# Kernel tuning notes

Hardware: AMD Instinct MI355X
Metric: run time of the kernel (lower is better)

## Reference

```python
import jax, jax.numpy as jnp
import numpy as np

NEG_INF = -1e30


def setup_inputs() -> dict:
    key = jax.random.key(0)
    kq, kk, kv, ks = jax.random.split(key, 4)
    B, H, S, D = 2, 16, 2048, 64
    return {
        "q": jax.random.normal(kq, (B, H, S, D), dtype=jnp.float32),
        "k": jax.random.normal(kk, (B, H, S, D), dtype=jnp.float32),
        "v": jax.random.normal(kv, (B, H, S, D), dtype=jnp.float32),
        "sink_weights": jax.random.normal(ks, (H,), dtype=jnp.float32),
        "sliding_window": 1024,
    }


def reference(q, k, v, sink_weights, sliding_window):
    """Sliding-window causal attention with a learnable attention-sink logit.

    Equivalent to FlexAttention.forward with sink_weights given: an extra kv
    position (the sink) is appended whose score is replaced by sink_weights[h]
    and whose value is zero -> it only adds mass to the softmax denominator.
    """
    B, H, S_q, D = q.shape
    S_kv = k.shape[2]
    scale = 1.0 / np.sqrt(D)

    # [B, H, S_q, S_kv] raw scores
    scores = jnp.einsum("bhqd,bhkd->bhqk", q, k) * scale

    q_idx = jnp.arange(S_q)[:, None]
    kv_idx = jnp.arange(S_kv)[None, :]
    keep = (kv_idx <= q_idx) & (q_idx - kv_idx <= sliding_window)  # [S_q, S_kv]
    scores = jnp.where(keep[None, None], scores, NEG_INF)

    # sink column: per-head learnable logit, always visible
    sink_col = jnp.broadcast_to(
        sink_weights[None, :, None, None], (B, H, S_q, 1)
    )
    logits = jnp.concatenate([scores, sink_col], axis=-1)  # [B,H,S_q,S_kv+1]

    probs = jax.nn.softmax(logits, axis=-1)
    # sink value is zero, so only the first S_kv prob columns hit v
    out = jnp.einsum("bhqk,bhkd->bhqd", probs[..., :S_kv], v)
    return out
```

## Files before the change

### kernel.cpp

```cpp
#include <hip/hip_runtime.h>


typedef __bf16 bf16x8 __attribute__((ext_vector_type(8)));
typedef __bf16 bf16x4 __attribute__((ext_vector_type(4)));
typedef float  f32x16 __attribute__((ext_vector_type(16)));

#define NT 256
#define NEG_BIG (-3.0e38f)

__device__ __forceinline__ int swz(int row, int gran) {
    return row * 64 + ((gran ^ ((row >> 1) & 7)) << 3);
}

__device__ __forceinline__ bf16x4 xswap32(bf16x4 v) {
    union { bf16x4 v; int i[2]; } u;
    u.v = v;
    u.i[0] = __shfl_xor(u.i[0], 32, 64);
    u.i[1] = __shfl_xor(u.i[1], 32, 64);
    return u.v;
}

__device__ const int SEG_N[24] = {3,2,2,2,2,1,2,1, 1,1,1,1,1,1,1,1, 1,1,1,1,1,1,1,1};
__device__ const int SEG_IT[24][3] = {
  {0,1,2},{2,3,0},{3,4,0},{4,5,0},{5,6,0},{6,0,0},{6,7,0},{7,0,0},
  {8,0,0},{8,0,0},{9,0,0},{9,0,0},{10,0,0},{10,0,0},{11,0,0},{11,0,0},
  {12,0,0},{12,0,0},{13,0,0},{13,0,0},{14,0,0},{14,0,0},{15,0,0},{15,0,0}};
__device__ const int SEG_J0[24][3] = {
  {0,0,0},{3,0,0},{6,0,0},{7,0,0},{6,0,0},{3,0,0},{12,0,0},{7,0,0},
  {0,0,0},{9,0,0},{0,0,0},{9,0,0},{0,0,0},{9,0,0},{0,0,0},{9,0,0},
  {0,0,0},{9,0,0},{0,0,0},{9,0,0},{0,0,0},{9,0,0},{0,0,0},{9,0,0}};
__device__ const int SEG_J1[24][3] = {
  {2,4,3},{6,6,0},{8,7,0},{10,6,0},{12,3,0},{12,0,0},{14,7,0},{16,0,0},
  {9,0,0},{18,0,0},{9,0,0},{18,0,0},{9,0,0},{18,0,0},{9,0,0},{18,0,0},
  {9,0,0},{18,0,0},{9,0,0},{18,0,0},{9,0,0},{18,0,0},{9,0,0},{18,0,0}};
__device__ const int SEG_SX[24][3] = {
  {0,0,0},{1,0,0},{1,0,0},{1,0,0},{1,0,0},{1,0,0},{2,0,0},{1,0,0},
  {0,0,0},{1,0,0},{0,0,0},{1,0,0},{0,0,0},{1,0,0},{0,0,0},{1,0,0},
  {0,0,0},{1,0,0},{0,0,0},{1,0,0},{0,0,0},{1,0,0},{0,0,0},{1,0,0}};
__device__ const int NSEG_ITEM[16] = {1,1,2,2,2,2,3,2, 2,2,2,2,2,2,2,2};

__global__ __launch_bounds__(NT, 3) void flex_r11_main(
    const float* __restrict__ Q, const float* __restrict__ K,
    const float* __restrict__ V, const float* __restrict__ SINKW,
    const int* __restrict__ SWIN, void* __restrict__ WS,
    float* __restrict__ OUT, const int H, const int S)
{
    const int t    = threadIdx.x;
    const int lane = t & 63;
    const int w    = t >> 6;
    const int c    = lane & 31;
    const int hl   = lane >> 5;
    const int W    = SWIN[0];
    const float scale = 0.125f;

    const int NBH = gridDim.x / 24;
    const int bh  = blockIdx.x / 24;
    const int b24 = blockIdx.x - bh * 24;
    const int h   = bh % H;
    const float sw = SINKW[h];

    __shared__ __align__(16) __bf16 k_lds[2][64 * 64];
    __shared__ __align__(16) __bf16 v_lds[2][64 * 64];

    const size_t basebh = (size_t)bh * S * 64;
    const float4* kp4 = (const float4*)(K + basebh);
    const float4* vp4 = (const float4*)(V + basebh);
    __bf16* O_ws  = (__bf16*)WS;
    float2* ml_ws = (float2*)((char*)WS + (size_t)NBH * 48 * 16384);

    const int dgi = t & 15;
    const int kgi = t >> 4;
    float4 kreg[4], vreg[4];

    const int ns = SEG_N[b24];

    {
        const int it0 = SEG_IT[b24][0];
        const int ktA0 = (2 * it0 - 16 > 0) ? (2 * it0 - 16) : 0;
        const int kt = ktA0 + SEG_J0[b24][0];
        #pragma unroll
        for (int i = 0; i < 4; ++i) kreg[i] = kp4[kt * 1024 + i * NT + t];
        #pragma unroll
        for (int kk = 0; kk < 4; ++kk) vreg[kk] = vp4[kt * 1024 + (4 * kgi + kk) * 16 + dgi];
        #pragma unroll
        for (int i = 0; i < 4; ++i) {
            const int flat = i * NT + t;
            const int key = flat >> 4, dd = flat & 15;
            float4 f = kreg[i];
            bf16x4 b = { (__bf16)f.x, (__bf16)f.y, (__bf16)f.z, (__bf16)f.w };
            *(bf16x4*)&k_lds[0][swz(key, dd >> 1) + (dd & 1) * 4] = b;
        }
        {
            float4 a0 = vreg[0], a1 = vreg[1], a2 = vreg[2], a3 = vreg[3];
            bf16x4 w0 = { (__bf16)a0.x, (__bf16)a1.x, (__bf16)a2.x, (__bf16)a3.x };
            bf16x4 w1 = { (__bf16)a0.y, (__bf16)a1.y, (__bf16)a2.y, (__bf16)a3.y };
            bf16x4 w2 = { (__bf16)a0.z, (__bf16)a1.z, (__bf16)a2.z, (__bf16)a3.z };
            bf16x4 w3 = { (__bf16)a0.w, (__bf16)a1.w, (__bf16)a2.w, (__bf16)a3.w };
            const int gv = kgi >> 1, ov = (kgi & 1) * 4;
            *(bf16x4*)&v_lds[0][swz(4 * dgi + 0, gv) + ov] = w0;
            *(bf16x4*)&v_lds[0][swz(4 * dgi + 1, gv) + ov] = w1;
            *(bf16x4*)&v_lds[0][swz(4 * dgi + 2, gv) + ov] = w2;
            *(bf16x4*)&v_lds[0][swz(4 * dgi + 3, gv) + ov] = w3;
        }
    }

    int par = 0;

    for (int s = 0; s < ns; ++s) {
        const int item = SEG_IT[b24][s];
        const int j0   = SEG_J0[b24][s];
        const int j1   = SEG_J1[b24][s];
        const int sidx = SEG_SX[b24][s];
        const int ktA  = (2 * item - 16 > 0) ? (2 * item - 16) : 0;
        const int qw0  = item * 128 + 32 * w;
        const int qi   = qw0 + c;

        bf16x8 bq[4];
        {
            const float4* qp4 = (const float4*)(Q + basebh + (size_t)qi * 64);
            #pragma unroll
            for (int ks = 0; ks < 4; ++ks) {
                float4 f0 = qp4[4 * ks + 2 * hl];
                float4 f1 = qp4[4 * ks + 2 * hl + 1];
                bq[ks][0] = (__bf16)(f0.x * scale); bq[ks][1] = (__bf16)(f0.y * scale);
                bq[ks][2] = (__bf16)(f0.z * scale); bq[ks][3] = (__bf16)(f0.w * scale);
                bq[ks][4] = (__bf16)(f1.x * scale); bq[ks][5] = (__bf16)(f1.y * scale);
                bq[ks][6] = (__bf16)(f1.z * scale); bq[ks][7] = (__bf16)(f1.w * scale);
            }
        }

        float mrun = (sidx == 0) ? sw : 0.0f;
        float lrun = (sidx == 0) ? 1.0f : 0.0f;
        f32x16 accO0, accO1;
        #pragma unroll
        for (int i = 0; i < 16; ++i) { accO0[i] = 0.0f; accO1[i] = 0.0f; }

        for (int j = j0; j < j1; ++j) {
            const int k0 = (ktA + j) * 64;

            __syncthreads();

            int nkt = -1;
            if (j + 1 < j1) nkt = ktA + j + 1;
            else if (s + 1 < ns) {
                const int it2 = SEG_IT[b24][s + 1];
                const int ktA2 = (2 * it2 - 16 > 0) ? (2 * it2 - 16) : 0;
                nkt = ktA2 + SEG_J0[b24][s + 1];
            }
            if (nkt >= 0) {
                #pragma unroll
                for (int i = 0; i < 4; ++i) kreg[i] = kp4[nkt * 1024 + i * NT + t];
                #pragma unroll
                for (int kk = 0; kk < 4; ++kk) vreg[kk] = vp4[nkt * 1024 + (4 * kgi + kk) * 16 + dgi];
            }

            const __bf16* kb = k_lds[par];
            const __bf16* vb = v_lds[par];
            f32x16 accS0, accS1;
            #pragma unroll
            for (int i = 0; i < 16; ++i) { accS0[i] = 0.0f; accS1[i] = 0.0f; }
            #pragma unroll
            for (int ks = 0; ks < 4; ++ks) {
                bf16x8 ka0 = *(const bf16x8*)&kb[swz(c,      2 * ks + hl)];
                bf16x8 ka1 = *(const bf16x8*)&kb[swz(32 + c, 2 * ks + hl)];
                accS0 = __builtin_amdgcn_mfma_f32_32x32x16_bf16(ka0, bq[ks], accS0, 0, 0, 0);
                accS1 = __builtin_amdgcn_mfma_f32_32x32x16_bf16(ka1, bq[ks], accS1, 0, 0, 0);
            }

            const bool interior = (k0 + 63 <= qw0) && (qw0 + 31 - k0 <= W);
            if (!interior) {
                #pragma unroll
                for (int rg = 0; rg < 16; ++rg) {
                    const int kb2 = (rg & 3) + 8 * (rg >> 2) + 4 * hl;
                    const int ki0 = k0 + kb2, ki1 = k0 + 32 + kb2;
                    if (!((ki0 <= qi) && (qi - ki0 <= W))) accS0[rg] = -1e30f;
                    if (!((ki1 <= qi) && (qi - ki1 <= W))) accS1[rg] = -1e30f;
                }
            }

            float mm[8];
            #pragma unroll
            for (int i = 0; i < 8; ++i)
                mm[i] = fmaxf(fmaxf(accS0[2*i], accS0[2*i+1]),
                              fmaxf(accS1[2*i], accS1[2*i+1]));
            float mx = fmaxf(fmaxf(fmaxf(mm[0], mm[1]), fmaxf(mm[2], mm[3])),
                             fmaxf(fmaxf(mm[4], mm[5]), fmaxf(mm[6], mm[7])));
            mx = fmaxf(mx, __shfl_xor(mx, 32, 64));

            #pragma unroll
            for (int i = 0; i < 16; ++i) accS0[i] = __expf(accS0[i] - mrun);
            #pragma unroll
            for (int i = 0; i < 16; ++i) accS1[i] = __expf(accS1[i] - mrun);

            float pp[8];
            #pragma unroll
            for (int i = 0; i < 8; ++i)
                pp[i] = (accS0[2*i] + accS0[2*i+1]) + (accS1[2*i] + accS1[2*i+1]);
            float ps = ((pp[0] + pp[1]) + (pp[2] + pp[3]))
                     + ((pp[4] + pp[5]) + (pp[6] + pp[7]));
            ps += __shfl_xor(ps, 32, 64);

            bf16x4 qA = { (__bf16)accS0[0],  (__bf16)accS0[1],  (__bf16)accS0[2],  (__bf16)accS0[3]  };
            bf16x4 qB = { (__bf16)accS0[4],  (__bf16)accS0[5],  (__bf16)accS0[6],  (__bf16)accS0[7]  };
            bf16x4 qC = { (__bf16)accS0[8],  (__bf16)accS0[9],  (__bf16)accS0[10], (__bf16)accS0[11] };
            bf16x4 qD = { (__bf16)accS0[12], (__bf16)accS0[13], (__bf16)accS0[14], (__bf16)accS0[15] };
            bf16x4 qE = { (__bf16)accS1[0],  (__bf16)accS1[1],  (__bf16)accS1[2],  (__bf16)accS1[3]  };
            bf16x4 qF = { (__bf16)accS1[4],  (__bf16)accS1[5],  (__bf16)accS1[6],  (__bf16)accS1[7]  };
            bf16x4 qG = { (__bf16)accS1[8],  (__bf16)accS1[9],  (__bf16)accS1[10], (__bf16)accS1[11] };
            bf16x4 qH = { (__bf16)accS1[12], (__bf16)accS1[13], (__bf16)accS1[14], (__bf16)accS1[15] };
            bf16x4 r0 = xswap32(hl ? qA : qB);
            bf16x4 r1 = xswap32(hl ? qC : qD);
            bf16x4 r2 = xswap32(hl ? qE : qF);
            bf16x4 r3 = xswap32(hl ? qG : qH);
            bf16x4 lo0 = hl ? r0 : qA, hi0 = hl ? qB : r0;
            bf16x4 lo1 = hl ? r1 : qC, hi1 = hl ? qD : r1;
            bf16x4 lo2 = hl ? r2 : qE, hi2 = hl ? qF : r2;
            bf16x4 lo3 = hl ? r3 : qG, hi3 = hl ? qH : r3;
            bf16x8 bp[4];
            #pragma unroll
            for (int e = 0; e < 4; ++e) {
                bp[0][e] = lo0[e]; bp[0][4+e] = hi0[e];
                bp[1][e] = lo1[e]; bp[1][4+e] = hi1[e];
                bp[2][e] = lo2[e]; bp[2][4+e] = hi2[e];
                bp[3][e] = lo3[e]; bp[3][4+e] = hi3[e];
            }

            #pragma unroll
            for (int ks = 0; ks < 4; ++ks) {
                bf16x8 va0 = *(const bf16x8*)&vb[swz(c,      2 * ks + hl)];
                bf16x8 va1 = *(const bf16x8*)&vb[swz(32 + c, 2 * ks + hl)];
                accO0 = __builtin_amdgcn_mfma_f32_32x32x16_bf16(va0, bp[ks], accO0, 0, 0, 0);
                accO1 = __builtin_amdgcn_mfma_f32_32x32x16_bf16(va1, bp[ks], accO1, 0, 0, 0);
            }

            const float mnew  = fmaxf(mrun, mx);
            const float alpha = __expf(mrun - mnew);
            lrun = (lrun + ps) * alpha;
            mrun = mnew;
            #pragma unroll
            for (int i = 0; i < 16; ++i) { accO0[i] *= alpha; accO1[i] *= alpha; }

            if (nkt >= 0) {
                const int np = par ^ 1;
                #pragma unroll
                for (int i = 0; i < 4; ++i) {
                    const int flat = i * NT + t;
                    const int key = flat >> 4, dd = flat & 15;
                    float4 f = kreg[i];
                    bf16x4 b = { (__bf16)f.x, (__bf16)f.y, (__bf16)f.z, (__bf16)f.w };
                    *(bf16x4*)&k_lds[np][swz(key, dd >> 1) + (dd & 1) * 4] = b;
                }
                float4 a0 = vreg[0], a1 = vreg[1], a2 = vreg[2], a3 = vreg[3];
                bf16x4 w0 = { (__bf16)a0.x, (__bf16)a1.x, (__bf16)a2.x, (__bf16)a3.x };
                bf16x4 w1 = { (__bf16)a0.y, (__bf16)a1.y, (__bf16)a2.y, (__bf16)a3.y };
                bf16x4 w2 = { (__bf16)a0.z, (__bf16)a1.z, (__bf16)a2.z, (__bf16)a3.z };
                bf16x4 w3 = { (__bf16)a0.w, (__bf16)a1.w, (__bf16)a2.w, (__bf16)a3.w };
                const int gv = kgi >> 1, ov = (kgi & 1) * 4;
                *(bf16x4*)&v_lds[np][swz(4 * dgi + 0, gv) + ov] = w0;
                *(bf16x4*)&v_lds[np][swz(4 * dgi + 1, gv) + ov] = w1;
                *(bf16x4*)&v_lds[np][swz(4 * dgi + 2, gv) + ov] = w2;
                *(bf16x4*)&v_lds[np][swz(4 * dgi + 3, gv) + ov] = w3;
            }
            par ^= 1;
        }

        if (item < 2) {
            const float inv = 1.0f / lrun;
            float* ob = OUT + basebh + (size_t)qi * 64;
            #pragma unroll
            for (int rg = 0; rg < 4; ++rg) {
                float4 f0 = { accO0[4*rg+0]*inv, accO0[4*rg+1]*inv,
                              accO0[4*rg+2]*inv, accO0[4*rg+3]*inv };
                float4 f1 = { accO1[4*rg+0]*inv, accO1[4*rg+1]*inv,
                              accO1[4*rg+2]*inv, accO1[4*rg+3]*inv };
                *(float4*)&ob[     8 * rg + 4 * hl] = f0;
                *(float4*)&ob[32 + 8 * rg + 4 * hl] = f1;
            }
        } else {
            const int slot = (bh * 16 + item) * 3 + sidx;
            const int qrel = 32 * w + c;
            if (hl == 0) ml_ws[(size_t)slot * 128 + qrel] = make_float2(mrun, lrun);
            __bf16* Os = O_ws + (size_t)slot * 8192 + (size_t)qrel * 64;
            #pragma unroll
            for (int qd = 0; qd < 4; ++qd) {
                const int d0 = 8 * qd + 4 * hl;
                bf16x4 b0 = { (__bf16)accO0[4*qd+0], (__bf16)accO0[4*qd+1],
                              (__bf16)accO0[4*qd+2], (__bf16)accO0[4*qd+3] };
                bf16x4 b1 = { (__bf16)accO1[4*qd+0], (__bf16)accO1[4*qd+1],
                              (__bf16)accO1[4*qd+2], (__bf16)accO1[4*qd+3] };
                *(bf16x4*)&Os[d0]      = b0;
                *(bf16x4*)&Os[32 + d0] = b1;
            }
        }
    }
}

__global__ __launch_bounds__(256) void flex_r11_combine(
    const void* __restrict__ WS, float* __restrict__ OUT, const int H, const int S)
{
    const int NBH  = gridDim.x / 14;
    const int bi   = blockIdx.x;
    const int bh   = bi / 14;
    const int item = 2 + (bi - bh * 14);
    const int ns   = NSEG_ITEM[item];
    const int t    = threadIdx.x;
    const int q    = t >> 1;
    const int half = t & 1;

    const __bf16* O_ws = (const __bf16*)WS;
    const float2* ml_ws = (const float2*)((const char*)WS + (size_t)NBH * 48 * 16384);
    const int base = (bh * 16 + item) * 3;

    float m[3], lv[3], a[3];
    float mst = NEG_BIG;
    for (int s = 0; s < ns; ++s) {
        float2 e = ml_ws[(size_t)(base + s) * 128 + q];
        m[s] = e.x; lv[s] = e.y;
        mst = fmaxf(mst, m[s]);
    }
    float lst = 0.0f;
    for (int s = 0; s < ns; ++s) { a[s] = __expf(m[s] - mst); lst += a[s] * lv[s]; }
    const float inv = 1.0f / lst;

    float acc[32];
    #pragma unroll
    for (int i = 0; i < 32; ++i) acc[i] = 0.0f;
    for (int s = 0; s < ns; ++s) {
        const __bf16* Os = O_ws + (size_t)(base + s) * 8192 + (size_t)q * 64 + 32 * half;
        const float as = a[s];
        #pragma unroll
        for (int v8 = 0; v8 < 4; ++v8) {
            bf16x8 o = *(const bf16x8*)&Os[8 * v8];
            #pragma unroll
            for (int jj = 0; jj < 8; ++jj) acc[8 * v8 + jj] += as * (float)o[jj];
        }
    }

    float* dst = OUT + (size_t)bh * S * 64 + (size_t)(item * 128 + q) * 64 + 32 * half;
    #pragma unroll
    for (int v4 = 0; v4 < 8; ++v4) {
        float4 f = { acc[4*v4+0] * inv, acc[4*v4+1] * inv,
                     acc[4*v4+2] * inv, acc[4*v4+3] * inv };
        *(float4*)&dst[4 * v4] = f;
    }
}

extern "C" void kernel_launch(void* const* d_in, const int* in_sizes, int n_in,
                              void* d_out, int out_size, void* d_ws, size_t ws_size,
                              hipStream_t stream) {
    const float* q     = (const float*)d_in[0];
    const float* k     = (const float*)d_in[1];
    const float* v     = (const float*)d_in[2];
    const float* sinkw = (const float*)d_in[3];
    const int*   swin  = (const int*)d_in[4];
    float* out = (float*)d_out;

    const int H = in_sizes[3];
    const int S = 2048;
    const int B = in_sizes[0] / (H * S * 64);
    const int NBH = B * H;

    flex_r11_main<<<dim3(NBH * 24), NT, 0, stream>>>(q, k, v, sinkw, swin, d_ws, out, H, S);
    flex_r11_combine<<<dim3(NBH * 14), 256, 0, stream>>>(d_ws, out, H, S);
}
```

Measured before the change: 141.5 us.

## Fuse split-KV combine into main kernel via atomic counter; switch to exp2 online softmax

Drops the separate combine kernel. The last segment block for each query item, found with an atomic counter in the workspace, now does the cross-segment merge inside the main kernel. Exponentials move to base 2 by folding log2(e) into the Q scale and the sink logit. The online-softmax update is also reworked to use the new running max before the exponent instead of a fixed reference. This saves a launch and the partials round trip, but adds a memset launch, fences, atomics and extra syncthreads, and the combining block takes on extra tail work.

Result: slower. 416.2 us (+194.1%).

```diff
diff --git a/kernel.cpp b/kernel.cpp
--- a/kernel.cpp
+++ b/kernel.cpp
@@ -7,6 +7,7 @@
 
 #define NT 256
 #define NEG_BIG (-3.0e38f)
+#define LOG2E 1.44269504089f
 
 __device__ __forceinline__ int swz(int row, int gran) {
     return row * 64 + ((gran ^ ((row >> 1) & 7)) << 3);
@@ -39,7 +40,7 @@
   {0,0,0},{1,0,0},{0,0,0},{1,0,0},{0,0,0},{1,0,0},{0,0,0},{1,0,0}};
 __device__ const int NSEG_ITEM[16] = {1,1,2,2,2,2,3,2, 2,2,2,2,2,2,2,2};
 
-__global__ __launch_bounds__(NT, 3) void flex_r11_main(
+__global__ __launch_bounds__(NT, 3) void flex_r13_main(
     const float* __restrict__ Q, const float* __restrict__ K,
     const float* __restrict__ V, const float* __restrict__ SINKW,
     const int* __restrict__ SWIN, void* __restrict__ WS,
@@ -51,22 +52,24 @@
     const int c    = lane & 31;
     const int hl   = lane >> 5;
     const int W    = SWIN[0];
-    const float scale = 0.125f;
+    const float qscale = 0.125f * LOG2E;
 
     const int NBH = gridDim.x / 24;
     const int bh  = blockIdx.x / 24;
     const int b24 = blockIdx.x - bh * 24;
     const int h   = bh % H;
-    const float sw = SINKW[h];
+    const float sw = SINKW[h] * LOG2E;
 
     __shared__ __align__(16) __bf16 k_lds[2][64 * 64];
     __shared__ __align__(16) __bf16 v_lds[2][64 * 64];
+    __shared__ int comb_flag;
 
     const size_t basebh = (size_t)bh * S * 64;
     const float4* kp4 = (const float4*)(K + basebh);
     const float4* vp4 = (const float4*)(V + basebh);
     __bf16* O_ws  = (__bf16*)WS;
     float2* ml_ws = (float2*)((char*)WS + (size_t)NBH * 48 * 16384);
+    int*    cnt_ws = (int*)((char*)WS + (size_t)NBH * 48 * 17408);
 
     const int dgi = t & 15;
     const int kgi = t >> 4;
@@ -122,14 +125,14 @@
             for (int ks = 0; ks < 4; ++ks) {
                 float4 f0 = qp4[4 * ks + 2 * hl];
                 float4 f1 = qp4[4 * ks + 2 * hl + 1];
-                bq[ks][0] = (__bf16)(f0.x * scale); bq[ks][1] = (__bf16)(f0.y * scale);
-                bq[ks][2] = (__bf16)(f0.z * scale); bq[ks][3] = (__bf16)(f0.w * scale);
-                bq[ks][4] = (__bf16)(f1.x * scale); bq[ks][5] = (__bf16)(f1.y * scale);
-                bq[ks][6] = (__bf16)(f1.z * scale); bq[ks][7] = (__bf16)(f1.w * scale);
-            }
-        }
-
-        float mrun = (sidx == 0) ? sw : 0.0f;
+                bq[ks][0] = (__bf16)(f0.x * qscale); bq[ks][1] = (__bf16)(f0.y * qscale);
+                bq[ks][2] = (__bf16)(f0.z * qscale); bq[ks][3] = (__bf16)(f0.w * qscale);
+                bq[ks][4] = (__bf16)(f1.x * qscale); bq[ks][5] = (__bf16)(f1.y * qscale);
+                bq[ks][6] = (__bf16)(f1.z * qscale); bq[ks][7] = (__bf16)(f1.w * qscale);
+            }
+        }
+
+        float mrun = (sidx == 0) ? sw : NEG_BIG;
         float lrun = (sidx == 0) ? 1.0f : 0.0f;
         f32x16 accO0, accO1;
         #pragma unroll
@@ -186,12 +189,12 @@
             float mx = fmaxf(fmaxf(fmaxf(mm[0], mm[1]), fmaxf(mm[2], mm[3])),
                              fmaxf(fmaxf(mm[4], mm[5]), fmaxf(mm[6], mm[7])));
             mx = fmaxf(mx, __shfl_xor(mx, 32, 64));
-
-            #pragma unroll
-            for (int i = 0; i < 16; ++i) accS0[i] = __expf(accS0[i] - mrun);
-            #pragma unroll
-            for (int i = 0; i < 16; ++i) accS1[i] = __expf(accS1[i] - mrun);
-
+            const float mnew  = fmaxf(mrun, mx);
+            const float alpha = exp2f(mrun - mnew);
+            #pragma unroll
+            for (int i = 0; i < 16; ++i) accS0[i] = exp2f(accS0[i] - mnew);
+            #pragma unroll
+            for (int i = 0; i < 16; ++i) accS1[i] = exp2f(accS1[i] - mnew);
             float pp[8];
             #pragma unroll
             for (int i = 0; i < 8; ++i)
@@ -199,6 +202,10 @@
             float ps = ((pp[0] + pp[1]) + (pp[2] + pp[3]))
                      + ((pp[4] + pp[5]) + (pp[6] + pp[7]));
             ps += __shfl_xor(ps, 32, 64);
+            lrun = lrun * alpha + ps;
+            mrun = mnew;
+            #pragma unroll
+            for (int i = 0; i < 16; ++i) { accO0[i] *= alpha; accO1[i] *= alpha; }
 
             bf16x4 qA = { (__bf16)accS0[0],  (__bf16)accS0[1],  (__bf16)accS0[2],  (__bf16)accS0[3]  };
             bf16x4 qB = { (__bf16)accS0[4],  (__bf16)accS0[5],  (__bf16)accS0[6],  (__bf16)accS0[7]  };
@@ -233,13 +240,6 @@
                 accO1 = __builtin_amdgcn_mfma_f32_32x32x16_bf16(va1, bp[ks], accO1, 0, 0, 0);
             }
 
-            const float mnew  = fmaxf(mrun, mx);
-            const float alpha = __expf(mrun - mnew);
-            lrun = (lrun + ps) * alpha;
-            mrun = mnew;
-            #pragma unroll
-            for (int i = 0; i < 16; ++i) { accO0[i] *= alpha; accO1[i] *= alpha; }
-
             if (nkt >= 0) {
                 const int np = par ^ 1;
                 #pragma unroll
@@ -291,57 +291,59 @@
                 *(bf16x4*)&Os[d0]      = b0;
                 *(bf16x4*)&Os[32 + d0] = b1;
             }
-        }
-    }
-}
-
-__global__ __launch_bounds__(256) void flex_r11_combine(
-    const void* __restrict__ WS, float* __restrict__ OUT, const int H, const int S)
-{
-    const int NBH  = gridDim.x / 14;
-    const int bi   = blockIdx.x;
-    const int bh   = bi / 14;
-    const int item = 2 + (bi - bh * 14);
-    const int ns   = NSEG_ITEM[item];
-    const int t    = threadIdx.x;
-    const int q    = t >> 1;
-    const int half = t & 1;
-
-    const __bf16* O_ws = (const __bf16*)WS;
-    const float2* ml_ws = (const float2*)((const char*)WS + (size_t)NBH * 48 * 16384);
-    const int base = (bh * 16 + item) * 3;
-
-    float m[3], lv[3], a[3];
-    float mst = NEG_BIG;
-    for (int s = 0; s < ns; ++s) {
-        float2 e = ml_ws[(size_t)(base + s) * 128 + q];
-        m[s] = e.x; lv[s] = e.y;
-        mst = fmaxf(mst, m[s]);
-    }
-    float lst = 0.0f;
-    for (int s = 0; s < ns; ++s) { a[s] = __expf(m[s] - mst); lst += a[s] * lv[s]; }
-    const float inv = 1.0f / lst;
-
-    float acc[32];
-    #pragma unroll
-    for (int i = 0; i < 32; ++i) acc[i] = 0.0f;
-    for (int s = 0; s < ns; ++s) {
-        const __bf16* Os = O_ws + (size_t)(base + s) * 8192 + (size_t)q * 64 + 32 * half;
-        const float as = a[s];
-        #pragma unroll
-        for (int v8 = 0; v8 < 4; ++v8) {
-            bf16x8 o = *(const bf16x8*)&Os[8 * v8];
-            #pragma unroll
-            for (int jj = 0; jj < 8; ++jj) acc[8 * v8 + jj] += as * (float)o[jj];
-        }
-    }
-
-    float* dst = OUT + (size_t)bh * S * 64 + (size_t)(item * 128 + q) * 64 + 32 * half;
-    #pragma unroll
-    for (int v4 = 0; v4 < 8; ++v4) {
-        float4 f = { acc[4*v4+0] * inv, acc[4*v4+1] * inv,
-                     acc[4*v4+2] * inv, acc[4*v4+3] * inv };
-        *(float4*)&dst[4 * v4] = f;
+
+            __threadfence();
+            if (t == 0)
+                comb_flag = (atomicAdd(&cnt_ws[bh * 16 + item], 1)
+                             == NSEG_ITEM[item] - 1);
+            __syncthreads();
+
+            if (comb_flag) {
+                __threadfence();
+                const int ns2  = NSEG_ITEM[item];
+                const int qq   = t >> 1;
+                const int half = t & 1;
+                const int base = (bh * 16 + item) * 3;
+
+                float m2[3], lv2[3], a2[3];
+                float mst = NEG_BIG;
+                for (int s2 = 0; s2 < ns2; ++s2) {
+                    float2 e = ml_ws[(size_t)(base + s2) * 128 + qq];
+                    m2[s2] = e.x; lv2[s2] = e.y;
+                    mst = fmaxf(mst, m2[s2]);
+                }
+                float lst = 0.0f;
+                for (int s2 = 0; s2 < ns2; ++s2) {
+                    a2[s2] = exp2f(m2[s2] - mst);
+                    lst += a2[s2] * lv2[s2];
+                }
+                const float inv = 1.0f / lst;
+
+                float acc[32];
+                #pragma unroll
+                for (int i = 0; i < 32; ++i) acc[i] = 0.0f;
+                for (int s2 = 0; s2 < ns2; ++s2) {
+                    const __bf16* Or = O_ws + (size_t)(base + s2) * 8192
+                                     + (size_t)qq * 64 + 32 * half;
+                    const float as = a2[s2];
+                    #pragma unroll
+                    for (int v8 = 0; v8 < 4; ++v8) {
+                        bf16x8 o = *(const bf16x8*)&Or[8 * v8];
+                        #pragma unroll
+                        for (int jj = 0; jj < 8; ++jj)
+                            acc[8 * v8 + jj] += as * (float)o[jj];
+                    }
+                }
+                float* dst = OUT + basebh + (size_t)(item * 128 + qq) * 64 + 32 * half;
+                #pragma unroll
+                for (int v4 = 0; v4 < 8; ++v4) {
+                    float4 f = { acc[4*v4+0] * inv, acc[4*v4+1] * inv,
+                                 acc[4*v4+2] * inv, acc[4*v4+3] * inv };
+                    *(float4*)&dst[4 * v4] = f;
+                }
+            }
+            __syncthreads();
+        }
     }
 }
 
@@ -360,6 +362,9 @@
     const int B = in_sizes[0] / (H * S * 64);
     const int NBH = B * H;
 
-    flex_r11_main<<<dim3(NBH * 24), NT, 0, stream>>>(q, k, v, sinkw, swin, d_ws, out, H, S);
-    flex_r11_combine<<<dim3(NBH * 14), 256, 0, stream>>>(d_ws, out, H, S);
+    hipMemsetAsync((char*)d_ws + (size_t)NBH * 48 * 17408, 0,
+                   NBH * 16 * sizeof(int), stream);
+
+    flex_r13_main<<<dim3(NBH * 24), NT, 0, stream>>>(q, k, v, sinkw, swin,
+                                                     d_ws, out, H, S);
 }
```
